# Kernel optimization log

Measured on AMD Instinct MI355X. Metric: run time of the kernel, lower is better.

## Reference

```python
import math
import jax, jax.numpy as jnp
import numpy as np

HEAD_NUM = 8
DIM = 512
D_K = DIM // HEAD_NUM  # 64
M_FEAT = 256
B, L = 4, 2048
STAB = 1e-5


def _orthogonal_gaussian(m, d, rng):
    num_squares = m // d
    blocks = []
    for _ in range(num_squares):
        q, _ = np.linalg.qr(rng.standard_normal((d, d)))
        blocks.append(q.T)
    rem = m - d * num_squares
    if rem:
        q, _ = np.linalg.qr(rng.standard_normal((d, d)))
        blocks.append(q.T[:rem])
    mat = np.concatenate(blocks, axis=0)
    mat = mat / math.sqrt(num_squares + rem / d)
    return mat.astype(np.float32)


def setup_inputs() -> dict:
    key = jax.random.key(0)
    ks = jax.random.split(key, 12)
    rng = np.random.default_rng(0)
    inp = {
        'query': jax.random.normal(ks[0], (B, L, DIM), jnp.float32),
        'key': jax.random.normal(ks[1], (B, L, DIM), jnp.float32),
        'value': jax.random.normal(ks[2], (B, L, DIM), jnp.float32),
        'proj': jnp.asarray(_orthogonal_gaussian(M_FEAT, D_K, rng)),  # [M, d_k]
        'w_q_w': jax.random.normal(ks[3], (DIM, DIM), jnp.float32) * 0.02,
        'w_q_b': jnp.zeros((DIM,), jnp.float32),
        'w_k_w': jax.random.normal(ks[4], (DIM, DIM), jnp.float32) * 0.02,
        'w_k_b': jnp.zeros((DIM,), jnp.float32),
        'w_v_w': jax.random.normal(ks[5], (DIM, DIM), jnp.float32) * 0.02,
        'w_v_b': jnp.zeros((DIM,), jnp.float32),
        'w_o_w': jax.random.normal(ks[6], (DIM, DIM), jnp.float32) * 0.02,
        'w_o_b': jnp.zeros((DIM,), jnp.float32),
    }
    return inp


def _relu_kernel(data, proj):
    # data: [B,L,H,D], proj: [M,D] -> [B,L,H,M]
    ratio = 1.0 / math.sqrt(proj.shape[0])
    return jax.nn.relu(ratio * jnp.einsum('blhd,md->blhm', data, proj)) + STAB


def _favor_causal(qp, kp, vs):
    # qp, kp: [L,B,H,M]; vs: [L,B,H,D] -> num [L,B,H,D], den [L,B,H]
    b, h, m = qp.shape[1], qp.shape[2], qp.shape[3]
    d = vs.shape[3]
    carry0 = (jnp.zeros((b, h, m, d), qp.dtype), jnp.zeros((b, h, m), qp.dtype))

    def step(carry, inp):
        s_kv, s_k = carry
        q_l, k_l, v_l = inp
        s_kv = s_kv + jnp.einsum('bhm,bhd->bhmd', k_l, v_l)
        s_k = s_k + k_l
        num = jnp.einsum('bhmd,bhm->bhd', s_kv, q_l)
        den = jnp.sum(q_l * s_k, axis=-1)
        return (s_kv, s_k), (num, den)

    _, (num, den) = jax.lax.scan(step, carry0, (qp, kp, vs))
    return num, den


def reference(query, key, value, proj, w_q_w, w_q_b, w_k_w, w_k_b, w_v_w, w_v_b, w_o_w, w_o_b):
    bsz = query.shape[0]
    q = (query @ w_q_w.T + w_q_b).reshape(bsz, -1, HEAD_NUM, D_K)
    k = (key @ w_k_w.T + w_k_b).reshape(bsz, -1, HEAD_NUM, D_K)
    v = (value @ w_v_w.T + w_v_b).reshape(bsz, -1, HEAD_NUM, D_K)
    qp = jnp.swapaxes(_relu_kernel(q, proj), 0, 1)  # [L,B,H,M]
    kp = jnp.swapaxes(_relu_kernel(k, proj), 0, 1)
    vs = jnp.swapaxes(v, 0, 1)                      # [L,B,H,D]
    num, den = _favor_causal(qp, kp, vs)
    attn = jnp.swapaxes(num, 0, 1) / jnp.swapaxes(den, 0, 1)[..., None]  # [B,L,H,D]
    attn = attn.reshape(bsz, -1, HEAD_NUM * D_K)
    return attn @ w_o_w.T + w_o_b
```

## Files before the change

kernel.cpp:

```cpp
#include <hip/hip_runtime.h>
#include <stdint.h>

#define B_ 4
#define L_ 2048
#define H_ 8
#define DK 64
#define M_ 256
#define DIM_ 512
#define NTOK (B_ * L_)
#define CHK 128
#define NC (L_ / CHK)
#define BH (B_ * H_)
#define RATIO 0.0625f
#define STABC 1e-5f

typedef unsigned short ushort_t;
typedef __attribute__((ext_vector_type(8))) short bf8v;
typedef __attribute__((ext_vector_type(4))) float f4v;

#define MFMA16(a, b, c) __builtin_amdgcn_mfma_f32_16x16x32_bf16(a, b, c, 0, 0, 0)

__device__ __forceinline__ ushort_t f2bf(float f) {
  uint32_t u = __float_as_uint(f);
  return (ushort_t)((u + 0x7fffu + ((u >> 16) & 1u)) >> 16);
}
__device__ __forceinline__ float bf2f(ushort_t u) { return __uint_as_float(((uint32_t)u) << 16); }

__device__ __forceinline__ void gll16(const void* g, void* l) {
  __builtin_amdgcn_global_load_lds((const __attribute__((address_space(1))) void*)g,
                                   (__attribute__((address_space(3))) void*)l, 16, 0, 0);
}

__device__ __forceinline__ bf8v ldfrag(const ushort_t* base, int row, int cb) {
  return *(const bf8v*)((const char*)base + row * 128 + (cb ^ ((row & 7) << 4)));
}
__device__ __forceinline__ bf8v ldfrag256(const ushort_t* base, int row, int cb) {
  return *(const bf8v*)((const char*)base + row * 256 + (cb ^ ((row & 7) << 4)));
}
__device__ __forceinline__ bf8v ldfrag512(const ushort_t* base, int row, int cb) {
  return *(const bf8v*)((const char*)base + row * 512 + (cb ^ ((row & 7) << 4)));
}

__global__ __launch_bounds__(256) void cvt_w(const float* __restrict__ wq, const float* __restrict__ wk,
                                             const float* __restrict__ wv, const float* __restrict__ wo,
                                             const float* __restrict__ pj, ushort_t* __restrict__ d) {
  int i = (blockIdx.x * 256 + threadIdx.x) * 8;
  const float* s;
  int off;
  if (i < 262144)       { s = wq; off = i; }
  else if (i < 524288)  { s = wk; off = i - 262144; }
  else if (i < 786432)  { s = wv; off = i - 524288; }
  else if (i < 1048576) { s = wo; off = i - 786432; }
  else                  { s = pj; off = i - 1048576; }
  float4 a = *(const float4*)(s + off);
  float4 b = *(const float4*)(s + off + 4);
  union { ushort_t u[8]; uint4 vv; } o;
  o.u[0] = f2bf(a.x); o.u[1] = f2bf(a.y); o.u[2] = f2bf(a.z); o.u[3] = f2bf(a.w);
  o.u[4] = f2bf(b.x); o.u[5] = f2bf(b.y); o.u[6] = f2bf(b.z); o.u[7] = f2bf(b.w);
  *(uint4*)(d + i) = o.vv;
}

__global__ __launch_bounds__(256) void qkvgemm_k(const float* __restrict__ q, const float* __restrict__ k,
                                                 const float* __restrict__ v, const ushort_t* __restrict__ Wc,
                                                 const float* __restrict__ bq, const float* __restrict__ bk,
                                                 const float* __restrict__ bv, ushort_t* __restrict__ XHq,
                                                 ushort_t* __restrict__ XHk, ushort_t* __restrict__ VT) {
  __shared__ char SB[65536];
  ushort_t* Tt = (ushort_t*)SB;
  const int z = blockIdx.z;
  const float* X = (z == 0) ? q : (z == 1) ? k : v;
  const ushort_t* Bw = Wc + (size_t)z * 262144;
  const float* bias = (z == 0) ? bq : (z == 1) ? bk : bv;
  const int tid = threadIdx.x, lane = tid & 63, w = tid >> 6;
  const int bm = blockIdx.x * 128, bn = blockIdx.y * 128;
  const int srow = w * 8 + (lane >> 3);
  const int scol = (((lane & 7) * 16) ^ ((lane >> 3) << 4)) >> 1;
  const int wr = (w >> 1) * 64, wc = (w & 1) * 64;
  const int fr = lane & 15, ks = lane >> 4, fq = lane >> 4;
  f4v acc[4][4] = {};
  {
#pragma unroll
    for (int i = 0; i < 4; ++i)
      gll16(Bw + (size_t)(bn + i * 32 + srow) * DIM_ + scol, SB + 32768 + i * 4096 + w * 1024);
#pragma unroll
    for (int i = 0; i < 4; ++i) {
      int e = tid + i * 256;
      int r = e >> 3, g = e & 7;
      const float* src = X + (size_t)(bm + r) * DIM_ + g * 8;
      float4 f0 = *(const float4*)src;
      float4 f1 = *(const float4*)(src + 4);
      union { ushort_t u[8]; bf8v v8; } pk;
      pk.u[0] = f2bf(f0.x); pk.u[1] = f2bf(f0.y); pk.u[2] = f2bf(f0.z); pk.u[3] = f2bf(f0.w);
      pk.u[4] = f2bf(f1.x); pk.u[5] = f2bf(f1.y); pk.u[6] = f2bf(f1.z); pk.u[7] = f2bf(f1.w);
      *(bf8v*)(SB + r * 128 + ((g * 16) ^ ((r & 7) << 4))) = pk.v8;
    }
  }
  __syncthreads();
  for (int t = 0; t < 8; ++t) {
    const ushort_t* curA = (const ushort_t*)(SB + (t & 1) * 16384);
    const ushort_t* curB = (const ushort_t*)(SB + 32768 + (t & 1) * 16384);
    char* nxtA = SB + ((t + 1) & 1) * 16384;
    char* nxtB = SB + 32768 + ((t + 1) & 1) * 16384;
    const int nk = (t + 1) * 64;
    float4 fA[4][2];
    if (t < 7) {
#pragma unroll
      for (int i = 0; i < 4; ++i) {
        int e = tid + i * 256;
        int r = e >> 3, g = e & 7;
        const float* src = X + (size_t)(bm + r) * DIM_ + nk + g * 8;
        fA[i][0] = *(const float4*)src;
        fA[i][1] = *(const float4*)(src + 4);
      }
#pragma unroll
      for (int i = 0; i < 4; ++i)
        gll16(Bw + (size_t)(bn + i * 32 + srow) * DIM_ + nk + scol, nxtB + i * 4096 + w * 1024);
    }
#pragma unroll
    for (int kk = 0; kk < 2; ++kk) {
      const int cb = kk * 64 + ks * 16;
      bf8v av[4], bv2[4];
#pragma unroll
      for (int m = 0; m < 4; ++m) av[m] = ldfrag(curA, wr + m * 16 + fr, cb);
#pragma unroll
      for (int n = 0; n < 4; ++n) bv2[n] = ldfrag(curB, wc + n * 16 + fr, cb);
#pragma unroll
      for (int m = 0; m < 4; ++m)
#pragma unroll
        for (int n = 0; n < 4; ++n) acc[m][n] = MFMA16(av[m], bv2[n], acc[m][n]);
    }
    if (t < 7) {
#pragma unroll
      for (int i = 0; i < 4; ++i) {
        int e = tid + i * 256;
        int r = e >> 3, g = e & 7;
        union { ushort_t u[8]; bf8v v8; } pk;
        pk.u[0] = f2bf(fA[i][0].x); pk.u[1] = f2bf(fA[i][0].y);
        pk.u[2] = f2bf(fA[i][0].z); pk.u[3] = f2bf(fA[i][0].w);
        pk.u[4] = f2bf(fA[i][1].x); pk.u[5] = f2bf(fA[i][1].y);
        pk.u[6] = f2bf(fA[i][1].z); pk.u[7] = f2bf(fA[i][1].w);
        *(bf8v*)(nxtA + r * 128 + ((g * 16) ^ ((r & 7) << 4))) = pk.v8;
      }
    }
    __syncthreads();
  }
  if (z == 2) {
#pragma unroll
    for (int m = 0; m < 4; ++m)
#pragma unroll
      for (int n = 0; n < 4; ++n) {
        int cl = wc + n * 16 + fr;
        float bsv = bias[bn + cl];
#pragma unroll
        for (int j = 0; j < 4; ++j) {
          int rl = wr + m * 16 + fq * 4 + j;
          Tt[cl * 136 + rl] = f2bf(acc[m][n][j] + bsv);
        }
      }
    __syncthreads();
    const int dl = tid >> 1, seg = tid & 1;
    const int c = bn + dl;
    const int bh2 = (bm >> 11) * 8 + (c >> 6);
    const int drow = c & 63;
    size_t vbase = ((size_t)(bh2 * 64 + drow)) * L_ + (bm & 2047) + seg * 64;
#pragma unroll
    for (int qq = 0; qq < 8; ++qq)
      *(uint4*)&VT[vbase + qq * 8] = *(const uint4*)&Tt[dl * 136 + seg * 64 + qq * 8];
  } else {
    ushort_t* Y = (z == 0) ? XHq : XHk;
#pragma unroll
    for (int m = 0; m < 4; ++m)
#pragma unroll
      for (int n = 0; n < 4; ++n) {
        int col = bn + wc + n * 16 + fr;
        float bsv = bias[col];
#pragma unroll
        for (int j = 0; j < 4; ++j) {
          int row = bm + wr + m * 16 + fq * 4 + j;
          Y[(size_t)row * DIM_ + col] = f2bf(acc[m][n][j] + bsv);
        }
      }
  }
}

__global__ __launch_bounds__(256) void cp2_k(const ushort_t* __restrict__ XHk, const ushort_t* __restrict__ P,
                                             const ushort_t* __restrict__ VT, ushort_t* __restrict__ S) {
  __shared__ ushort_t Ps[256 * 64];
  __shared__ ushort_t Xs[128 * 64];
  __shared__ ushort_t Kt[256 * 128];
  const int ci = blockIdx.x, bh = blockIdx.y;
  const int b = bh >> 3, h = bh & 7;
  const int tid = threadIdx.x, lane = tid & 63, w = tid >> 6;
  const int srow = w * 8 + (lane >> 3);
  const int scol = (((lane & 7) * 16) ^ ((lane >> 3) << 4)) >> 1;
  const int fr = lane & 15, ks = lane >> 4, fq = lane >> 4;
  const int l0 = ci * CHK;
#pragma unroll
  for (int i = 0; i < 8; ++i)
    gll16(P + (size_t)(i * 32 + srow) * 64 + scol, (char*)Ps + i * 4096 + w * 1024);
#pragma unroll
  for (int i = 0; i < 4; ++i)
    gll16(XHk + (size_t)(b * L_ + l0 + i * 32 + srow) * DIM_ + h * 64 + scol, (char*)Xs + i * 4096 + w * 1024);
  __syncthreads();
  {
    f4v acc[4][8] = {};
#pragma unroll
    for (int kk = 0; kk < 2; ++kk) {
      const int cb = kk * 64 + ks * 16;
      bf8v av[4], bv[8];
#pragma unroll
      for (int m = 0; m < 4; ++m) av[m] = ldfrag(Ps, w * 64 + m * 16 + fr, cb);
#pragma unroll
      for (int n = 0; n < 8; ++n) bv[n] = ldfrag(Xs, n * 16 + fr, cb);
#pragma unroll
      for (int m = 0; m < 4; ++m)
#pragma unroll
        for (int n = 0; n < 8; ++n) acc[m][n] = MFMA16(av[m], bv[n], acc[m][n]);
    }
#pragma unroll
    for (int m = 0; m < 4; ++m)
#pragma unroll
      for (int n = 0; n < 8; ++n) {
        const int mb = w * 64 + m * 16 + fq * 4;
        const int ll = n * 16 + fr;
#pragma unroll
        for (int j = 0; j < 4; ++j) {
          float v = fmaxf(RATIO * acc[m][n][j], 0.f) + STABC;
          *(ushort_t*)((char*)Kt + (mb + j) * 256 + ((ll * 2) ^ (((mb + j) & 7) << 4))) = f2bf(v);
        }
      }
  }
  __syncthreads();
  f4v accS[5][4] = {};
  for (int kt = 0; kt < 2; ++kt) {
#pragma unroll
    for (int i = 0; i < 2; ++i)
      gll16(VT + ((size_t)bh * 64 + i * 32 + srow) * L_ + l0 + kt * 64 + scol, (char*)Xs + i * 4096 + w * 1024);
    if (tid < 32) ((uint32_t*)Xs)[2048 + tid] = 0x3f803f80u;
    __syncthreads();
#pragma unroll
    for (int kk = 0; kk < 2; ++kk) {
      const int cbA = kk * 64 + ks * 16;
      const int cbK = kt * 128 + kk * 64 + ks * 16;
      bf8v av[5], bv[4];
#pragma unroll
      for (int a = 0; a < 5; ++a) av[a] = ldfrag(Xs, a * 16 + fr, cbA);
#pragma unroll
      for (int n = 0; n < 4; ++n) bv[n] = ldfrag256(Kt, w * 64 + n * 16 + fr, cbK);
#pragma unroll
      for (int a = 0; a < 5; ++a)
#pragma unroll
        for (int n = 0; n < 4; ++n) accS[a][n] = MFMA16(av[a], bv[n], accS[a][n]);
    }
    __syncthreads();
  }
  const size_t base = ((size_t)bh * NC + ci) * 65;
#pragma unroll
  for (int a = 0; a < 5; ++a)
#pragma unroll
    for (int n = 0; n < 4; ++n)
#pragma unroll
      for (int j = 0; j < 4; ++j) {
        int row = a * 16 + fq * 4 + j;
        if (row < 65) S[(base + row) * M_ + w * 64 + n * 16 + fr] = f2bf(accS[a][n][j]);
      }
}

__global__ __launch_bounds__(256) void prefix2_k(ushort_t* __restrict__ S) {
  const int g = blockIdx.x * 256 + threadIdx.x;
  const int bh = g / 2080, r = g - bh * 2080;
  ushort_t* base = S + (size_t)bh * (NC * 65 * M_) + (size_t)r * 8;
  uint4 v[16];
#pragma unroll
  for (int ci = 0; ci < NC; ++ci) v[ci] = *(const uint4*)(base + (size_t)ci * (65 * M_));
  float c[8] = {};
#pragma unroll
  for (int ci = 0; ci < NC; ++ci) {
    union { uint4 u; ushort_t s[8]; } in, out;
    in.u = v[ci];
#pragma unroll
    for (int e = 0; e < 8; ++e) {
      float t = bf2f(in.s[e]);
      out.s[e] = f2bf(c[e]);
      c[e] += t;
    }
    *(uint4*)(base + (size_t)ci * (65 * M_)) = out.u;
  }
}

__global__ __launch_bounds__(512) void qkout4_k(const ushort_t* __restrict__ XHq, const ushort_t* __restrict__ XHk,
                                                const ushort_t* __restrict__ P, const ushort_t* __restrict__ VT,
                                                const ushort_t* __restrict__ S, ushort_t* __restrict__ attn) {
  __shared__ char LB[147456];
  ushort_t* Qp  = (ushort_t*)LB;
  ushort_t* Pj  = (ushort_t*)(LB + 65536);
  ushort_t* Kps = (ushort_t*)(LB + 98304);
  ushort_t* R2  = (ushort_t*)(LB + 114688);
  ushort_t* Xk  = (ushort_t*)(LB + 131072);
  const int ci = blockIdx.x, bh = blockIdx.y;
  const int b = bh >> 3, h = bh & 7;
  const int tid = threadIdx.x, lane = tid & 63, w = tid >> 6;
  const int srow = w * 8 + (lane >> 3);
  const int scol = (((lane & 7) * 16) ^ ((lane >> 3) << 4)) >> 1;
  const int fr = lane & 15, ks = lane >> 4, fq = lane >> 4;
  const int l0 = ci * CHK;
  const size_t tokb = (size_t)b * L_ + l0;
  const size_t sbase = ((size_t)bh * NC + ci) * 65;
#pragma unroll
  for (int i = 0; i < 4; ++i)
    gll16(P + (size_t)(i * 64 + srow) * 64 + scol, (char*)Pj + i * 8192 + w * 1024);
#pragma unroll
  for (int i = 0; i < 2; ++i) {
    gll16(XHq + (tokb + i * 64 + srow) * DIM_ + h * 64 + scol, (char*)R2 + i * 8192 + w * 1024);
    gll16(XHk + (tokb + i * 64 + srow) * DIM_ + h * 64 + scol, (char*)Xk + i * 8192 + w * 1024);
  }
  __syncthreads();
  {
    f4v accF[2][8] = {};
#pragma unroll
    for (int kk = 0; kk < 2; ++kk) {
      const int cb = kk * 64 + ks * 16;
      bf8v av[2], bv[8];
#pragma unroll
      for (int m = 0; m < 2; ++m) av[m] = ldfrag(Pj, w * 32 + m * 16 + fr, cb);
#pragma unroll
      for (int n = 0; n < 8; ++n) bv[n] = ldfrag(R2, n * 16 + fr, cb);
#pragma unroll
      for (int m = 0; m < 2; ++m)
#pragma unroll
        for (int n = 0; n < 8; ++n) accF[m][n] = MFMA16(av[m], bv[n], accF[m][n]);
    }
#pragma unroll
    for (int m = 0; m < 2; ++m)
#pragma unroll
      for (int n = 0; n < 8; ++n) {
        const int mb = w * 32 + m * 16 + fq * 4;
        const int ll = n * 16 + fr;
        ushort_t bvv[4];
#pragma unroll
        for (int j = 0; j < 4; ++j)
          bvv[j] = f2bf(fmaxf(RATIO * accF[m][n][j], 0.f) + STABC);
        uint2 pk;
        pk.x = (uint32_t)bvv[0] | ((uint32_t)bvv[1] << 16);
        pk.y = (uint32_t)bvv[2] | ((uint32_t)bvv[3] << 16);
        *(uint2*)((char*)Qp + ll * 512 + ((mb * 2) ^ ((ll & 7) << 4))) = pk;
      }
  }
  __syncthreads();
  const int qr = (w & 3) * 32, qc = (w >> 2) * 64;
  const int orow = w * 16;
  f4v accA[2][4] = {};
  f4v acc2[5] = {};
  for (int kt = 0; kt < 4; ++kt) {
    gll16(S + (sbase + srow) * M_ + kt * 64 + scol, (char*)R2 + w * 1024);
    if (tid < 32)
      ((uint32_t*)R2)[2048 + tid] = ((const uint32_t*)(S + (sbase + 64) * M_ + kt * 64))[tid];
    {
      const int fi = w >> 1, tf0 = (w & 1) * 4;
      f4v accK[4] = {};
#pragma unroll
      for (int kk = 0; kk < 2; ++kk) {
        const int cb = kk * 64 + ks * 16;
        bf8v ap = ldfrag(Pj, kt * 64 + fi * 16 + fr, cb);
        bf8v bx[4];
#pragma unroll
        for (int t2 = 0; t2 < 4; ++t2) bx[t2] = ldfrag(Xk, (tf0 + t2) * 16 + fr, cb);
#pragma unroll
        for (int t2 = 0; t2 < 4; ++t2) accK[t2] = MFMA16(ap, bx[t2], accK[t2]);
      }
#pragma unroll
      for (int t2 = 0; t2 < 4; ++t2) {
        const int tt = (tf0 + t2) * 16 + fr;
        const int fl = fi * 16 + fq * 4;
#pragma unroll
        for (int j = 0; j < 4; ++j) {
          float v = fmaxf(RATIO * accK[t2][j], 0.f) + STABC;
          *(ushort_t*)((char*)Kps + tt * 128 + (((fl + j) * 2) ^ ((tt & 7) << 4))) = f2bf(v);
        }
      }
    }
    __syncthreads();
#pragma unroll
    for (int kk = 0; kk < 2; ++kk) {
      const int cb = kk * 64 + ks * 16;
      const int cbQ = kt * 128 + cb;
      bf8v aq[2], bk_[4], a2, sv[5];
#pragma unroll
      for (int m = 0; m < 2; ++m) aq[m] = ldfrag512(Qp, qr + m * 16 + fr, cbQ);
#pragma unroll
      for (int n = 0; n < 4; ++n) bk_[n] = ldfrag(Kps, qc + n * 16 + fr, cb);
#pragma unroll
      for (int m = 0; m < 2; ++m)
#pragma unroll
        for (int n = 0; n < 4; ++n) accA[m][n] = MFMA16(aq[m], bk_[n], accA[m][n]);
      a2 = ldfrag512(Qp, orow + fr, cbQ);
#pragma unroll
      for (int n = 0; n < 5; ++n) sv[n] = ldfrag(R2, n * 16 + fr, cb);
#pragma unroll
      for (int n = 0; n < 5; ++n) acc2[n] = MFMA16(a2, sv[n], acc2[n]);
    }
    __syncthreads();
  }
#pragma unroll
  for (int m = 0; m < 2; ++m)
#pragma unroll
    for (int n = 0; n < 4; ++n)
#pragma unroll
      for (int j = 0; j < 4; ++j) {
        int row = qr + m * 16 + fq * 4 + j;
        int col = qc + n * 16 + fr;
        float v = (col <= row) ? accA[m][n][j] : 0.f;
        *(ushort_t*)((char*)Pj + row * 256 + ((col * 2) ^ ((row & 7) << 4))) = f2bf(v);
      }
  __syncthreads();
  for (int kt2 = 0; kt2 < 2; ++kt2) {
    gll16(VT + ((size_t)bh * 64 + srow) * L_ + l0 + kt2 * 64 + scol, (char*)R2 + w * 1024);
    if (tid < 32) ((uint32_t*)R2)[2048 + tid] = 0x3f803f80u;
    __syncthreads();
#pragma unroll
    for (int kk = 0; kk < 2; ++kk) {
      const int cb = kk * 64 + ks * 16;
      bf8v a3, sv[5];
      a3 = ldfrag256(Pj, orow + fr, kt2 * 128 + cb);
#pragma unroll
      for (int n = 0; n < 5; ++n) sv[n] = ldfrag(R2, n * 16 + fr, cb);
#pragma unroll
      for (int n = 0; n < 5; ++n) acc2[n] = MFMA16(a3, sv[n], acc2[n]);
    }
    __syncthreads();
  }
  float dinv[4];
#pragma unroll
  for (int j = 0; j < 4; ++j) {
    float den = __shfl(acc2[4][j], (lane & 48));
    dinv[j] = 1.f / den;
  }
#pragma unroll
  for (int n = 0; n < 4; ++n)
#pragma unroll
    for (int j = 0; j < 4; ++j) {
      int l = orow + fq * 4 + j;
      int col = h * 64 + n * 16 + fr;
      attn[(tokb + l) * DIM_ + col] = f2bf(acc2[n][j] * dinv[j]);
    }
}

__global__ __launch_bounds__(256) void gemmo_k(const ushort_t* __restrict__ A, const ushort_t* __restrict__ Bw,
                                               const float* __restrict__ bias, float* __restrict__ Y) {
  __shared__ char SB[49152];
  const int tid = threadIdx.x, lane = tid & 63, w = tid >> 6;
  const int bm = blockIdx.x * 128, bn = blockIdx.y * 64;
  const int srow = w * 8 + (lane >> 3);
  const int scol = (((lane & 7) * 16) ^ ((lane >> 3) << 4)) >> 1;
  const int wr = (w >> 1) * 64, wc = (w & 1) * 32;
  const int fr = lane & 15, ks = lane >> 4, fq = lane >> 4;
  f4v acc[4][2] = {};
#pragma unroll
  for (int i = 0; i < 4; ++i)
    gll16(A + (size_t)(bm + i * 32 + srow) * DIM_ + scol, SB + i * 4096 + w * 1024);
#pragma unroll
  for (int i = 0; i < 2; ++i)
    gll16(Bw + (size_t)(bn + i * 32 + srow) * DIM_ + scol, SB + 32768 + i * 4096 + w * 1024);
  __syncthreads();
  for (int t = 0; t < 8; ++t) {
    const ushort_t* curA = (const ushort_t*)(SB + (t & 1) * 16384);
    const ushort_t* curB = (const ushort_t*)(SB + 32768 + (t & 1) * 8192);
    char* nxtA = SB + ((t + 1) & 1) * 16384;
    char* nxtB = SB + 32768 + ((t + 1) & 1) * 8192;
    const int nk = (t + 1) * 64;
    if (t < 7) {
#pragma unroll
      for (int i = 0; i < 4; ++i)
        gll16(A + (size_t)(bm + i * 32 + srow) * DIM_ + nk + scol, nxtA + i * 4096 + w * 1024);
#pragma unroll
      for (int i = 0; i < 2; ++i)
        gll16(Bw + (size_t)(bn + i * 32 + srow) * DIM_ + nk + scol, nxtB + i * 4096 + w * 1024);
    }
#pragma unroll
    for (int kk = 0; kk < 2; ++kk) {
      const int cb = kk * 64 + ks * 16;
      bf8v av[4], bv[2];
#pragma unroll
      for (int m = 0; m < 4; ++m) av[m] = ldfrag(curA, wr + m * 16 + fr, cb);
#pragma unroll
      for (int n = 0; n < 2; ++n) bv[n] = ldfrag(curB, wc + n * 16 + fr, cb);
#pragma unroll
      for (int m = 0; m < 4; ++m)
#pragma unroll
        for (int n = 0; n < 2; ++n) acc[m][n] = MFMA16(av[m], bv[n], acc[m][n]);
    }
    __syncthreads();
  }
#pragma unroll
  for (int m = 0; m < 4; ++m)
#pragma unroll
    for (int n = 0; n < 2; ++n) {
      int col = bn + wc + n * 16 + fr;
      float bsv = bias[col];
#pragma unroll
      for (int j = 0; j < 4; ++j) {
        int row = bm + wr + m * 16 + fq * 4 + j;
        Y[(size_t)row * DIM_ + col] = acc[m][n][j] + bsv;
      }
    }
}

extern "C" void kernel_launch(void* const* d_in, const int* in_sizes, int n_in,
                              void* d_out, int out_size, void* d_ws, size_t ws_size,
                              hipStream_t stream) {
  const float* query = (const float*)d_in[0];
  const float* key   = (const float*)d_in[1];
  const float* value = (const float*)d_in[2];
  const float* proj  = (const float*)d_in[3];
  const float* wq = (const float*)d_in[4];
  const float* bq = (const float*)d_in[5];
  const float* wk = (const float*)d_in[6];
  const float* bk = (const float*)d_in[7];
  const float* wv = (const float*)d_in[8];
  const float* bv = (const float*)d_in[9];
  const float* wo = (const float*)d_in[10];
  const float* bo = (const float*)d_in[11];

  char* ws = (char*)d_ws;
  ushort_t* Wc   = (ushort_t*)(ws);
  ushort_t* XHq  = (ushort_t*)(ws + 2129920);
  ushort_t* XHk  = (ushort_t*)(ws + 10518528);
  ushort_t* VT   = (ushort_t*)(ws + 18907136);
  ushort_t* Skv  = (ushort_t*)(ws + 27295744);
  ushort_t* attb = (ushort_t*)(ws + 44335104);
  const ushort_t* Wo = Wc + 786432;
  const ushort_t* Pc = Wc + 1048576;

  dim3 blk(256);
  cvt_w<<<520, blk, 0, stream>>>(wq, wk, wv, wo, proj, Wc);
  qkvgemm_k<<<dim3(64, 4, 3), blk, 0, stream>>>(query, key, value, Wc, bq, bk, bv, XHq, XHk, VT);
  cp2_k<<<dim3(NC, BH), blk, 0, stream>>>(XHk, Pc, VT, Skv);
  prefix2_k<<<260, blk, 0, stream>>>(Skv);
  qkout4_k<<<dim3(NC, BH), dim3(512), 0, stream>>>(XHq, XHk, Pc, VT, Skv, attb);
  gemmo_k<<<dim3(64, 8), blk, 0, stream>>>(attb, Wo, bo, (float*)d_out);
}
```

Measured before the change: 97.73 us.

## Widen QKV and output GEMM tiles to 128x256 with 512-thread single-buffered blocks

Both the QKV projection GEMM and the output GEMM now use 512-thread blocks with a 128x256 output tile, up from 128x128 and 128x64. Each wave still computes a 64x64 sub-tile. Double buffering with register prefetch is dropped in favour of a single shared-memory stage, with a barrier before and after compute. The V-transpose epilogue is split into two halves to fit the smaller shared buffer. The larger tiles are meant to raise operand reuse and cut redundant A-tile loads and conversions, but grid size falls to 384 and 128 blocks and load latency is no longer overlapped with compute.

```diff
diff --git a/kernel.cpp b/kernel.cpp
--- a/kernel.cpp
+++ b/kernel.cpp
@@ -60,33 +60,34 @@
   *(uint4*)(d + i) = o.vv;
 }
 
-__global__ __launch_bounds__(256) void qkvgemm_k(const float* __restrict__ q, const float* __restrict__ k,
+__global__ __launch_bounds__(512) void qkvgemm_k(const float* __restrict__ q, const float* __restrict__ k,
                                                  const float* __restrict__ v, const ushort_t* __restrict__ Wc,
                                                  const float* __restrict__ bq, const float* __restrict__ bk,
                                                  const float* __restrict__ bv, ushort_t* __restrict__ XHq,
                                                  ushort_t* __restrict__ XHk, ushort_t* __restrict__ VT) {
-  __shared__ char SB[65536];
+  __shared__ char SB[49152];
   ushort_t* Tt = (ushort_t*)SB;
   const int z = blockIdx.z;
   const float* X = (z == 0) ? q : (z == 1) ? k : v;
   const ushort_t* Bw = Wc + (size_t)z * 262144;
   const float* bias = (z == 0) ? bq : (z == 1) ? bk : bv;
   const int tid = threadIdx.x, lane = tid & 63, w = tid >> 6;
-  const int bm = blockIdx.x * 128, bn = blockIdx.y * 128;
-  const int srow = w * 8 + (lane >> 3);
+  const int bm = blockIdx.x * 128, bn = blockIdx.y * 256;
   const int scol = (((lane & 7) * 16) ^ ((lane >> 3) << 4)) >> 1;
-  const int wr = (w >> 1) * 64, wc = (w & 1) * 64;
   const int fr = lane & 15, ks = lane >> 4, fq = lane >> 4;
+  const int wr = (w >> 2) * 64, wc = (w & 3) * 64;
   f4v acc[4][4] = {};
-  {
+  for (int t = 0; t < 8; ++t) {
+    const int k0 = t * 64;
 #pragma unroll
     for (int i = 0; i < 4; ++i)
-      gll16(Bw + (size_t)(bn + i * 32 + srow) * DIM_ + scol, SB + 32768 + i * 4096 + w * 1024);
-#pragma unroll
-    for (int i = 0; i < 4; ++i) {
-      int e = tid + i * 256;
+      gll16(Bw + (size_t)(bn + w * 32 + i * 8 + (lane >> 3)) * DIM_ + k0 + scol,
+            SB + 16384 + w * 4096 + i * 1024);
+#pragma unroll
+    for (int i = 0; i < 2; ++i) {
+      int e = tid + i * 512;
       int r = e >> 3, g = e & 7;
-      const float* src = X + (size_t)(bm + r) * DIM_ + g * 8;
+      const float* src = X + (size_t)(bm + r) * DIM_ + k0 + g * 8;
       float4 f0 = *(const float4*)src;
       float4 f1 = *(const float4*)(src + 4);
       union { ushort_t u[8]; bf8v v8; } pk;
@@ -94,78 +95,50 @@
       pk.u[4] = f2bf(f1.x); pk.u[5] = f2bf(f1.y); pk.u[6] = f2bf(f1.z); pk.u[7] = f2bf(f1.w);
       *(bf8v*)(SB + r * 128 + ((g * 16) ^ ((r & 7) << 4))) = pk.v8;
     }
-  }
-  __syncthreads();
-  for (int t = 0; t < 8; ++t) {
-    const ushort_t* curA = (const ushort_t*)(SB + (t & 1) * 16384);
-    const ushort_t* curB = (const ushort_t*)(SB + 32768 + (t & 1) * 16384);
-    char* nxtA = SB + ((t + 1) & 1) * 16384;
-    char* nxtB = SB + 32768 + ((t + 1) & 1) * 16384;
-    const int nk = (t + 1) * 64;
-    float4 fA[4][2];
-    if (t < 7) {
-#pragma unroll
-      for (int i = 0; i < 4; ++i) {
-        int e = tid + i * 256;
-        int r = e >> 3, g = e & 7;
-        const float* src = X + (size_t)(bm + r) * DIM_ + nk + g * 8;
-        fA[i][0] = *(const float4*)src;
-        fA[i][1] = *(const float4*)(src + 4);
-      }
-#pragma unroll
-      for (int i = 0; i < 4; ++i)
-        gll16(Bw + (size_t)(bn + i * 32 + srow) * DIM_ + nk + scol, nxtB + i * 4096 + w * 1024);
-    }
+    __syncthreads();
 #pragma unroll
     for (int kk = 0; kk < 2; ++kk) {
       const int cb = kk * 64 + ks * 16;
       bf8v av[4], bv2[4];
 #pragma unroll
-      for (int m = 0; m < 4; ++m) av[m] = ldfrag(curA, wr + m * 16 + fr, cb);
-#pragma unroll
-      for (int n = 0; n < 4; ++n) bv2[n] = ldfrag(curB, wc + n * 16 + fr, cb);
+      for (int m = 0; m < 4; ++m) av[m] = ldfrag((const ushort_t*)SB, wr + m * 16 + fr, cb);
+#pragma unroll
+      for (int n = 0; n < 4; ++n) bv2[n] = ldfrag((const ushort_t*)(SB + 16384), wc + n * 16 + fr, cb);
 #pragma unroll
       for (int m = 0; m < 4; ++m)
 #pragma unroll
         for (int n = 0; n < 4; ++n) acc[m][n] = MFMA16(av[m], bv2[n], acc[m][n]);
     }
-    if (t < 7) {
-#pragma unroll
-      for (int i = 0; i < 4; ++i) {
-        int e = tid + i * 256;
-        int r = e >> 3, g = e & 7;
-        union { ushort_t u[8]; bf8v v8; } pk;
-        pk.u[0] = f2bf(fA[i][0].x); pk.u[1] = f2bf(fA[i][0].y);
-        pk.u[2] = f2bf(fA[i][0].z); pk.u[3] = f2bf(fA[i][0].w);
-        pk.u[4] = f2bf(fA[i][1].x); pk.u[5] = f2bf(fA[i][1].y);
-        pk.u[6] = f2bf(fA[i][1].z); pk.u[7] = f2bf(fA[i][1].w);
-        *(bf8v*)(nxtA + r * 128 + ((g * 16) ^ ((r & 7) << 4))) = pk.v8;
-      }
-    }
     __syncthreads();
   }
   if (z == 2) {
-#pragma unroll
-    for (int m = 0; m < 4; ++m)
-#pragma unroll
-      for (int n = 0; n < 4; ++n) {
-        int cl = wc + n * 16 + fr;
-        float bsv = bias[bn + cl];
-#pragma unroll
-        for (int j = 0; j < 4; ++j) {
-          int rl = wr + m * 16 + fq * 4 + j;
-          Tt[cl * 136 + rl] = f2bf(acc[m][n][j] + bsv);
-        }
-      }
-    __syncthreads();
-    const int dl = tid >> 1, seg = tid & 1;
-    const int c = bn + dl;
-    const int bh2 = (bm >> 11) * 8 + (c >> 6);
-    const int drow = c & 63;
-    size_t vbase = ((size_t)(bh2 * 64 + drow)) * L_ + (bm & 2047) + seg * 64;
-#pragma unroll
-    for (int qq = 0; qq < 8; ++qq)
-      *(uint4*)&VT[vbase + qq * 8] = *(const uint4*)&Tt[dl * 136 + seg * 64 + qq * 8];
+    for (int hh = 0; hh < 2; ++hh) {
+      if (((w & 3) >> 1) == hh) {
+        const int wcl = wc - hh * 128;
+#pragma unroll
+        for (int m = 0; m < 4; ++m)
+#pragma unroll
+          for (int n = 0; n < 4; ++n) {
+            int cl = wcl + n * 16 + fr;
+            float bsv = bias[bn + wc + n * 16 + fr];
+#pragma unroll
+            for (int j = 0; j < 4; ++j) {
+              int rl = wr + m * 16 + fq * 4 + j;
+              Tt[cl * 136 + rl] = f2bf(acc[m][n][j] + bsv);
+            }
+          }
+      }
+      __syncthreads();
+      const int dl = tid >> 2, seg = tid & 3;
+      const int c = bn + hh * 128 + dl;
+      const int bh2 = (bm >> 11) * 8 + (c >> 6);
+      const int drow = c & 63;
+      size_t vbase = ((size_t)(bh2 * 64 + drow)) * L_ + (bm & 2047) + seg * 32;
+#pragma unroll
+      for (int qq = 0; qq < 4; ++qq)
+        *(uint4*)&VT[vbase + qq * 8] = *(const uint4*)&Tt[dl * 136 + seg * 32 + qq * 8];
+      __syncthreads();
+    }
   } else {
     ushort_t* Y = (z == 0) ? XHq : XHk;
 #pragma unroll
@@ -445,56 +418,45 @@
     }
 }
 
-__global__ __launch_bounds__(256) void gemmo_k(const ushort_t* __restrict__ A, const ushort_t* __restrict__ Bw,
+__global__ __launch_bounds__(512) void gemmo_k(const ushort_t* __restrict__ A, const ushort_t* __restrict__ Bw,
                                                const float* __restrict__ bias, float* __restrict__ Y) {
   __shared__ char SB[49152];
   const int tid = threadIdx.x, lane = tid & 63, w = tid >> 6;
-  const int bm = blockIdx.x * 128, bn = blockIdx.y * 64;
-  const int srow = w * 8 + (lane >> 3);
+  const int bm = blockIdx.x * 128, bn = blockIdx.y * 256;
   const int scol = (((lane & 7) * 16) ^ ((lane >> 3) << 4)) >> 1;
-  const int wr = (w >> 1) * 64, wc = (w & 1) * 32;
   const int fr = lane & 15, ks = lane >> 4, fq = lane >> 4;
-  f4v acc[4][2] = {};
-#pragma unroll
-  for (int i = 0; i < 4; ++i)
-    gll16(A + (size_t)(bm + i * 32 + srow) * DIM_ + scol, SB + i * 4096 + w * 1024);
-#pragma unroll
-  for (int i = 0; i < 2; ++i)
-    gll16(Bw + (size_t)(bn + i * 32 + srow) * DIM_ + scol, SB + 32768 + i * 4096 + w * 1024);
-  __syncthreads();
+  const int wr = (w >> 2) * 64, wc = (w & 3) * 64;
+  f4v acc[4][4] = {};
   for (int t = 0; t < 8; ++t) {
-    const ushort_t* curA = (const ushort_t*)(SB + (t & 1) * 16384);
-    const ushort_t* curB = (const ushort_t*)(SB + 32768 + (t & 1) * 8192);
-    char* nxtA = SB + ((t + 1) & 1) * 16384;
-    char* nxtB = SB + 32768 + ((t + 1) & 1) * 8192;
-    const int nk = (t + 1) * 64;
-    if (t < 7) {
-#pragma unroll
-      for (int i = 0; i < 4; ++i)
-        gll16(A + (size_t)(bm + i * 32 + srow) * DIM_ + nk + scol, nxtA + i * 4096 + w * 1024);
-#pragma unroll
-      for (int i = 0; i < 2; ++i)
-        gll16(Bw + (size_t)(bn + i * 32 + srow) * DIM_ + nk + scol, nxtB + i * 4096 + w * 1024);
-    }
+    const int k0 = t * 64;
+#pragma unroll
+    for (int i = 0; i < 2; ++i)
+      gll16(A + (size_t)(bm + w * 16 + i * 8 + (lane >> 3)) * DIM_ + k0 + scol,
+            SB + w * 2048 + i * 1024);
+#pragma unroll
+    for (int i = 0; i < 4; ++i)
+      gll16(Bw + (size_t)(bn + w * 32 + i * 8 + (lane >> 3)) * DIM_ + k0 + scol,
+            SB + 16384 + w * 4096 + i * 1024);
+    __syncthreads();
 #pragma unroll
     for (int kk = 0; kk < 2; ++kk) {
       const int cb = kk * 64 + ks * 16;
-      bf8v av[4], bv[2];
-#pragma unroll
-      for (int m = 0; m < 4; ++m) av[m] = ldfrag(curA, wr + m * 16 + fr, cb);
-#pragma unroll
-      for (int n = 0; n < 2; ++n) bv[n] = ldfrag(curB, wc + n * 16 + fr, cb);
+      bf8v av[4], bv[4];
+#pragma unroll
+      for (int m = 0; m < 4; ++m) av[m] = ldfrag((const ushort_t*)SB, wr + m * 16 + fr, cb);
+#pragma unroll
+      for (int n = 0; n < 4; ++n) bv[n] = ldfrag((const ushort_t*)(SB + 16384), wc + n * 16 + fr, cb);
 #pragma unroll
       for (int m = 0; m < 4; ++m)
 #pragma unroll
-        for (int n = 0; n < 2; ++n) acc[m][n] = MFMA16(av[m], bv[n], acc[m][n]);
+        for (int n = 0; n < 4; ++n) acc[m][n] = MFMA16(av[m], bv[n], acc[m][n]);
     }
     __syncthreads();
   }
 #pragma unroll
   for (int m = 0; m < 4; ++m)
 #pragma unroll
-    for (int n = 0; n < 2; ++n) {
+    for (int n = 0; n < 4; ++n) {
       int col = bn + wc + n * 16 + fr;
       float bsv = bias[col];
 #pragma unroll
@@ -533,9 +495,9 @@
 
   dim3 blk(256);
   cvt_w<<<520, blk, 0, stream>>>(wq, wk, wv, wo, proj, Wc);
-  qkvgemm_k<<<dim3(64, 4, 3), blk, 0, stream>>>(query, key, value, Wc, bq, bk, bv, XHq, XHk, VT);
+  qkvgemm_k<<<dim3(64, 2, 3), dim3(512), 0, stream>>>(query, key, value, Wc, bq, bk, bv, XHq, XHk, VT);
   cp2_k<<<dim3(NC, BH), blk, 0, stream>>>(XHk, Pc, VT, Skv);
   prefix2_k<<<260, blk, 0, stream>>>(Skv);
   qkout4_k<<<dim3(NC, BH), dim3(512), 0, stream>>>(XHq, XHk, Pc, VT, Skv, attb);
-  gemmo_k<<<dim3(64, 8), blk, 0, stream>>>(attb, Wo, bo, (float*)d_out);
-}
+  gemmo_k<<<dim3(64, 2), dim3(512), 0, stream>>>(attb, Wo, bo, (float*)d_out);
+}
```

Result: no change. 99.21 us (+1.5%).
